# Kernel tuning notes

Measured on AMD Instinct MI355X. Metric: run time of the kernel, lower is better.

Reference implementation:

```python
import jax, jax.numpy as jnp
import numpy as np

INTEGRAL_RESOLUTION = 0.03  # matches self.integral_resolution

S, H, E, G, F = 4096, 3, 512, 3334, 1  # samples, heads, max events, grid points, formulas


def setup_inputs() -> dict:
    key = jax.random.key(0)
    k1, k2, k3, k4, k5, k6 = jax.random.split(key, 6)
    event_features = jax.random.uniform(k1, (S, H, E, F), dtype=jnp.float32)
    event_mask = jax.random.randint(k2, (S, H, E), 0, 2).astype(bool)
    grid_features = jax.random.uniform(k3, (S, H, G, F), dtype=jnp.float32)
    weights = jax.random.normal(k4, (H, F), dtype=jnp.float32)
    bases = jax.random.normal(k5, (H,), dtype=jnp.float32)
    effects = jnp.ones((H, F), dtype=jnp.float32)  # formula effect is +/-1
    return {
        "event_features": event_features,
        "event_mask": event_mask,
        "grid_features": grid_features,
        "weights": weights,
        "bases": bases,
        "effects": effects,
    }


def reference(event_features, event_mask, grid_features, weights, bases, effects):
    # intensity(t, h) = exp(base_h + sum_f w_{h,f} * feature_f(t) * effect_{h,f})
    w_eff = weights * effects  # [H, F]
    # log-intensity at event times: [S, H, E]
    ev_logit = bases[None, :, None] + jnp.einsum('shef,hf->she', event_features, w_eff)
    # log-intensity on the integral grid: [S, H, G]
    gr_logit = bases[None, :, None] + jnp.einsum('shgf,hf->shg', grid_features, w_eff)
    # sum of log(intensity) over valid events (log(exp(x)) = x)
    log_sum = jnp.sum(jnp.where(event_mask, ev_logit, jnp.zeros((), ev_logit.dtype)))
    # Riemann integral of intensity over [0, T_max]
    integral = jnp.asarray(INTEGRAL_RESOLUTION, gr_logit.dtype) * jnp.sum(jnp.exp(gr_logit))
    return log_sum - integral
```

## Files before the change

kernel.cpp:

```cpp
#include <hip/hip_runtime.h>

constexpr int S = 4096;
constexpr int H = 3;
constexpr int E = 512;
constexpr int G = 3334;
constexpr float RES = 0.03f;

__global__ __launch_bounds__(256) void logic_model_kernel(
    const float* __restrict__ ev,
    const int*   __restrict__ mask,
    const float* __restrict__ gr,
    const float* __restrict__ w,
    const float* __restrict__ bases,
    const float* __restrict__ eff,
    float* __restrict__ out)
{
    const float b0 = bases[0], b1 = bases[1], b2 = bases[2];
    const float w0 = w[0] * eff[0], w1 = w[1] * eff[1], w2 = w[2] * eff[2];

    const int tid = blockIdx.x * blockDim.x + threadIdx.x;
    const int nthreads = gridDim.x * blockDim.x;

    float acc_ev = 0.f;
    const int nf4 = S * H * E / 4;
    const float4* ev4 = (const float4*)ev;
    const int4*   m4  = (const int4*)mask;
    for (int i = tid; i < nf4; i += nthreads) {
        float4 x = ev4[i];
        int4   m = m4[i];
        int row = i >> 7;
        int h = row % 3;
        float bb = (h == 0) ? b0 : ((h == 1) ? b1 : b2);
        float ww = (h == 0) ? w0 : ((h == 1) ? w1 : w2);
        if (m.x) acc_ev += bb + ww * x.x;
        if (m.y) acc_ev += bb + ww * x.y;
        if (m.z) acc_ev += bb + ww * x.z;
        if (m.w) acc_ev += bb + ww * x.w;
    }

    float acc_gr = 0.f;
    const int nf2 = S * H * G / 2;
    const float2* gr2 = (const float2*)gr;
    for (int i = tid; i < nf2; i += nthreads) {
        float2 y = gr2[i];
        int row = i / 1667;
        int h = row % 3;
        float bb = (h == 0) ? b0 : ((h == 1) ? b1 : b2);
        float ww = (h == 0) ? w0 : ((h == 1) ? w1 : w2);
        acc_gr += __expf(bb + ww * y.x) + __expf(bb + ww * y.y);
    }

    float v = acc_ev - RES * acc_gr;

    #pragma unroll
    for (int off = 32; off > 0; off >>= 1)
        v += __shfl_down(v, off, 64);

    __shared__ float sdata[4];
    const int wave = threadIdx.x >> 6;
    const int lane = threadIdx.x & 63;
    if (lane == 0) sdata[wave] = v;
    __syncthreads();
    if (threadIdx.x == 0) {
        float t = sdata[0] + sdata[1] + sdata[2] + sdata[3];
        atomicAdd(out, t);
    }
}

extern "C" void kernel_launch(void* const* d_in, const int* in_sizes, int n_in,
                              void* d_out, int out_size, void* d_ws, size_t ws_size,
                              hipStream_t stream) {
    const float* ev    = (const float*)d_in[0];
    const int*   mask  = (const int*)  d_in[1];
    const float* gr    = (const float*)d_in[2];
    const float* w     = (const float*)d_in[3];
    const float* bases = (const float*)d_in[4];
    const float* eff   = (const float*)d_in[5];
    float* out = (float*)d_out;

    hipMemsetAsync(out, 0, sizeof(float), stream);

    logic_model_kernel<<<2048, 256, 0, stream>>>(ev, mask, gr, w, bases, eff, out);
}
```

Measured before the change: 284.4 us.

## Fully unroll grid-stride loops with float4 loads and software-prefetched batches

```diff
diff --git a/kernel.cpp b/kernel.cpp
--- a/kernel.cpp
+++ b/kernel.cpp
@@ -5,6 +5,34 @@
 constexpr int E = 512;
 constexpr int G = 3334;
 constexpr float RES = 0.03f;
+
+constexpr int NBLK = 2048;
+constexpr int NTHR = NBLK * 256;
+constexpr int NF4E = S * H * E / 4;
+constexpr int NF4G = S * H * G / 4;
+constexpr int SLOTS = 20;
+constexpr int LAST_VALID = NF4G - (SLOTS - 1) * NTHR;
+
+__device__ __forceinline__ float quad_exp(int fidx, float4 y,
+                                          float b0, float b1, float b2,
+                                          float w0, float w1, float w2) {
+    int j = fidx * 4;
+    int q = j / G;
+    int r = j - q * G;
+    int m = q - (q / 3) * 3;
+    int hB = (m == 2) ? 0 : (m + 1);
+    float bbA = (m == 0) ? b0 : ((m == 1) ? b1 : b2);
+    float wwA = (m == 0) ? w0 : ((m == 1) ? w1 : w2);
+    float bbB = (hB == 0) ? b0 : ((hB == 1) ? b1 : b2);
+    float wwB = (hB == 0) ? w0 : ((hB == 1) ? w1 : w2);
+    int lim = G - r;
+    float s;
+    s  = __expf(bbA + wwA * y.x);
+    s += __expf(((1 >= lim) ? bbB : bbA) + ((1 >= lim) ? wwB : wwA) * y.y);
+    s += __expf(((2 >= lim) ? bbB : bbA) + ((2 >= lim) ? wwB : wwA) * y.z);
+    s += __expf(((3 >= lim) ? bbB : bbA) + ((3 >= lim) ? wwB : wwA) * y.w);
+    return s;
+}
 
 __global__ __launch_bounds__(256) void logic_model_kernel(
     const float* __restrict__ ev,
@@ -19,17 +47,26 @@
     const float w0 = w[0] * eff[0], w1 = w[1] * eff[1], w2 = w[2] * eff[2];
 
     const int tid = blockIdx.x * blockDim.x + threadIdx.x;
-    const int nthreads = gridDim.x * blockDim.x;
+
+    const float4* ev4 = (const float4*)ev;
+    const int4*   m4  = (const int4*)mask;
+    const float4* gr4 = (const float4*)gr;
+
+    float4 x0 = ev4[tid], x1 = ev4[tid + NTHR], x2 = ev4[tid + 2 * NTHR];
+    int4   a0 = m4[tid],  a1 = m4[tid + NTHR],  a2 = m4[tid + 2 * NTHR];
+
+    float4 cur[4];
+    #pragma unroll
+    for (int u = 0; u < 4; ++u) cur[u] = gr4[tid + u * NTHR];
 
     float acc_ev = 0.f;
-    const int nf4 = S * H * E / 4;
-    const float4* ev4 = (const float4*)ev;
-    const int4*   m4  = (const int4*)mask;
-    for (int i = tid; i < nf4; i += nthreads) {
-        float4 x = ev4[i];
-        int4   m = m4[i];
+    #pragma unroll
+    for (int k = 0; k < 3; ++k) {
+        int i = tid + k * NTHR;
+        float4 x = (k == 0) ? x0 : ((k == 1) ? x1 : x2);
+        int4   m = (k == 0) ? a0 : ((k == 1) ? a1 : a2);
         int row = i >> 7;
-        int h = row % 3;
+        int h = row - (row / 3) * 3;
         float bb = (h == 0) ? b0 : ((h == 1) ? b1 : b2);
         float ww = (h == 0) ? w0 : ((h == 1) ? w1 : w2);
         if (m.x) acc_ev += bb + ww * x.x;
@@ -39,15 +76,31 @@
     }
 
     float acc_gr = 0.f;
-    const int nf2 = S * H * G / 2;
-    const float2* gr2 = (const float2*)gr;
-    for (int i = tid; i < nf2; i += nthreads) {
-        float2 y = gr2[i];
-        int row = i / 1667;
-        int h = row % 3;
-        float bb = (h == 0) ? b0 : ((h == 1) ? b1 : b2);
-        float ww = (h == 0) ? w0 : ((h == 1) ? w1 : w2);
-        acc_gr += __expf(bb + ww * y.x) + __expf(bb + ww * y.y);
+    #pragma unroll
+    for (int b = 1; b < 5; ++b) {
+        float4 nxt[4];
+        #pragma unroll
+        for (int u = 0; u < 4; ++u) {
+            int slot = 4 * b + u;
+            int idx = tid + slot * NTHR;
+            if (slot == SLOTS - 1) idx = min(idx, NF4G - 1);
+            nxt[u] = gr4[idx];
+        }
+        #pragma unroll
+        for (int u = 0; u < 4; ++u)
+            acc_gr += quad_exp(tid + (4 * (b - 1) + u) * NTHR, cur[u],
+                               b0, b1, b2, w0, w1, w2);
+        #pragma unroll
+        for (int u = 0; u < 4; ++u) cur[u] = nxt[u];
+    }
+    #pragma unroll
+    for (int u = 0; u < 3; ++u)
+        acc_gr += quad_exp(tid + (16 + u) * NTHR, cur[u],
+                           b0, b1, b2, w0, w1, w2);
+    {
+        int idx = min(tid + 19 * NTHR, NF4G - 1);
+        float t = quad_exp(idx, cur[3], b0, b1, b2, w0, w1, w2);
+        acc_gr += (tid < LAST_VALID) ? t : 0.f;
     }
 
     float v = acc_ev - RES * acc_gr;
@@ -73,12 +126,12 @@
     const float* ev    = (const float*)d_in[0];
     const int*   mask  = (const int*)  d_in[1];
     const float* gr    = (const float*)d_in[2];
-    const float* w     = (const float*)d_in[3];
+    const float* wgt   = (const float*)d_in[3];
     const float* bases = (const float*)d_in[4];
     const float* eff   = (const float*)d_in[5];
     float* out = (float*)d_out;
 
     hipMemsetAsync(out, 0, sizeof(float), stream);
 
-    logic_model_kernel<<<2048, 256, 0, stream>>>(ev, mask, gr, w, bases, eff, out);
+    logic_model_kernel<<<NBLK, 256, 0, stream>>>(ev, mask, gr, wgt, bases, eff, out);
 }
```

Result: faster. 273.2 us (-3.9%).

## Assign two rows per block with unrolled float4 grid loads and exp2

Applied to the files above, without the earlier changes.

```diff
diff --git a/kernel.cpp b/kernel.cpp
--- a/kernel.cpp
+++ b/kernel.cpp
@@ -5,6 +5,25 @@
 constexpr int E = 512;
 constexpr int G = 3334;
 constexpr float RES = 0.03f;
+constexpr float LOG2E = 1.44269504088896340736f;
+
+constexpr int BT   = 256;
+constexpr int NBLK = S * H / 2;
+constexpr int GF4  = 2 * G / 4;
+constexpr int GFULL = GF4 / BT;
+constexpr int GTAIL = GF4 - GFULL * BT;
+
+typedef float f4_t __attribute__((ext_vector_type(4)));
+typedef int   i4_t __attribute__((ext_vector_type(4)));
+
+template <typename T>
+__device__ __forceinline__ T ntload(const T* p) {
+#if __has_builtin(__builtin_nontemporal_load)
+    return __builtin_nontemporal_load(p);
+#else
+    return *p;
+#endif
+}
 
 __global__ __launch_bounds__(256) void logic_model_kernel(
     const float* __restrict__ ev,
@@ -17,37 +36,61 @@
 {
     const float b0 = bases[0], b1 = bases[1], b2 = bases[2];
     const float w0 = w[0] * eff[0], w1 = w[1] * eff[1], w2 = w[2] * eff[2];
+    const float c0 = b0 * LOG2E, c1 = b1 * LOG2E, c2 = b2 * LOG2E;
+    const float v0 = w0 * LOG2E, v1 = w1 * LOG2E, v2 = w2 * LOG2E;
 
-    const int tid = blockIdx.x * blockDim.x + threadIdx.x;
-    const int nthreads = gridDim.x * blockDim.x;
+    const int t = threadIdx.x;
+    const int b = blockIdx.x;
+
+    const int r2b = (2 * b) % 3;
+    const int h0 = r2b;
+    const int h1 = (r2b == 2) ? 0 : r2b + 1;
+    const float cr0 = (h0 == 0) ? c0 : ((h0 == 1) ? c1 : c2);
+    const float vr0 = (h0 == 0) ? v0 : ((h0 == 1) ? v1 : v2);
+    const float cr1 = (h1 == 0) ? c0 : ((h1 == 1) ? c1 : c2);
+    const float vr1 = (h1 == 0) ? v0 : ((h1 == 1) ? v1 : v2);
+
+    const f4_t* gr4 = (const f4_t*)gr;
+    const f4_t* ev4 = (const f4_t*)ev;
+    const i4_t* m4  = (const i4_t*)mask;
 
     float acc_ev = 0.f;
-    const int nf4 = S * H * E / 4;
-    const float4* ev4 = (const float4*)ev;
-    const int4*   m4  = (const int4*)mask;
-    for (int i = tid; i < nf4; i += nthreads) {
-        float4 x = ev4[i];
-        int4   m = m4[i];
-        int row = i >> 7;
-        int h = row % 3;
-        float bb = (h == 0) ? b0 : ((h == 1) ? b1 : b2);
-        float ww = (h == 0) ? w0 : ((h == 1) ? w1 : w2);
+    {
+        f4_t x = ntload(ev4 + (size_t)b * BT + t);
+        i4_t m = ntload(m4  + (size_t)b * BT + t);
+        const int he = (t < 128) ? h0 : h1;
+        const float bb = (he == 0) ? b0 : ((he == 1) ? b1 : b2);
+        const float ww = (he == 0) ? w0 : ((he == 1) ? w1 : w2);
         if (m.x) acc_ev += bb + ww * x.x;
         if (m.y) acc_ev += bb + ww * x.y;
         if (m.z) acc_ev += bb + ww * x.z;
         if (m.w) acc_ev += bb + ww * x.w;
     }
 
+    const int gbase = b * GF4;
     float acc_gr = 0.f;
-    const int nf2 = S * H * G / 2;
-    const float2* gr2 = (const float2*)gr;
-    for (int i = tid; i < nf2; i += nthreads) {
-        float2 y = gr2[i];
-        int row = i / 1667;
-        int h = row % 3;
-        float bb = (h == 0) ? b0 : ((h == 1) ? b1 : b2);
-        float ww = (h == 0) ? w0 : ((h == 1) ? w1 : w2);
-        acc_gr += __expf(bb + ww * y.x) + __expf(bb + ww * y.y);
+    #pragma unroll
+    for (int k = 0; k < GFULL; ++k) {
+        const int l = t + k * BT;
+        f4_t y = ntload(gr4 + gbase + l);
+        const int j = 4 * l;
+        float cA, vA;
+        cA = (j     < G) ? cr0 : cr1;  vA = (j     < G) ? vr0 : vr1;
+        acc_gr += exp2f(cA + vA * y.x);
+        cA = (j + 1 < G) ? cr0 : cr1;  vA = (j + 1 < G) ? vr0 : vr1;
+        acc_gr += exp2f(cA + vA * y.y);
+        cA = (j + 2 < G) ? cr0 : cr1;  vA = (j + 2 < G) ? vr0 : vr1;
+        acc_gr += exp2f(cA + vA * y.z);
+        cA = (j + 3 < G) ? cr0 : cr1;  vA = (j + 3 < G) ? vr0 : vr1;
+        acc_gr += exp2f(cA + vA * y.w);
+    }
+    if (t < GTAIL) {
+        const int l = t + GFULL * BT;
+        f4_t y = ntload(gr4 + gbase + l);
+        acc_gr += exp2f(cr1 + vr1 * y.x);
+        acc_gr += exp2f(cr1 + vr1 * y.y);
+        acc_gr += exp2f(cr1 + vr1 * y.z);
+        acc_gr += exp2f(cr1 + vr1 * y.w);
     }
 
     float v = acc_ev - RES * acc_gr;
@@ -62,8 +105,8 @@
     if (lane == 0) sdata[wave] = v;
     __syncthreads();
     if (threadIdx.x == 0) {
-        float t = sdata[0] + sdata[1] + sdata[2] + sdata[3];
-        atomicAdd(out, t);
+        float s = sdata[0] + sdata[1] + sdata[2] + sdata[3];
+        atomicAdd(out, s);
     }
 }
 
@@ -73,12 +116,12 @@
     const float* ev    = (const float*)d_in[0];
     const int*   mask  = (const int*)  d_in[1];
     const float* gr    = (const float*)d_in[2];
-    const float* w     = (const float*)d_in[3];
+    const float* wgt   = (const float*)d_in[3];
     const float* bases = (const float*)d_in[4];
     const float* eff   = (const float*)d_in[5];
     float* out = (float*)d_out;
 
     hipMemsetAsync(out, 0, sizeof(float), stream);
 
-    logic_model_kernel<<<2048, 256, 0, stream>>>(ev, mask, gr, w, bases, eff, out);
+    logic_model_kernel<<<NBLK, BT, 0, stream>>>(ev, mask, gr, wgt, bases, eff, out);
 }
```

Result: slower. 304.3 us (+7.0%).
